# Performance work log

Hardware: AMD Instinct MI355X
Metric: run time of the kernel (lower is better)

The kernel has to match this reference:

```python
import jax, jax.numpy as jnp
import numpy as np
from jax import lax

T, B, I, H = 512, 128, 512, 1024  # seq_len, batch, n_input, n_hidden


def setup_inputs() -> dict:
    key = jax.random.key(0)
    ks = jax.random.split(key, 7)
    si, sh = I ** -0.5, H ** -0.5  # scaled init so tanh does not saturate
    return {
        "x":   jax.random.normal(ks[0], (T, B, I), jnp.float32),
        "Wi0": jax.random.normal(ks[1], (I, H), jnp.float32) * si,
        "Wh0": jax.random.normal(ks[2], (H, H), jnp.float32) * sh,
        "Ws0": jax.random.normal(ks[3], (I, H), jnp.float32) * si,
        "Wi1": jax.random.normal(ks[4], (H, H), jnp.float32) * sh,
        "Wh1": jax.random.normal(ks[5], (H, H), jnp.float32) * sh,
        "Ws1": jax.random.normal(ks[6], (I, H), jnp.float32) * si,
    }


def _wrnn_layer(pre, Wh):
    # pre: [L, B, H] precomputed non-recurrent projections (input-proj + scaled-input-proj)
    # h_t = tanh(pre[t] + h_{t-1} @ Wh)   -- true sequential recurrence
    def step(h, p):
        h = jnp.tanh(p + h @ Wh)
        return h, h
    h0 = jnp.zeros(pre.shape[1:], pre.dtype)
    _, out = lax.scan(step, h0, pre)
    return out  # [L, B, H]


def reference(x, Wi0, Wh0, Ws0, Wi1, Wh1, Ws1):
    # Layer 0: scale = 1, so scaled_x == x and input == x; index offset 0.
    # Hoist both non-recurrent matmuls into one big GEMM over all timesteps.
    pre0 = jnp.einsum('tbi,ih->tbh', x, Wi0 + Ws0)  # same as x@Wi0 + x@Ws0
    out0 = _wrnn_layer(pre0, Wh0)                   # [T, B, H]

    # Layer 1: scale = 2 moving average of x (length T-1); input = out0 at index i+1.
    sx1 = (x[:-1] + x[1:]) * 0.5                    # [T-1, B, I]
    pre1 = (jnp.einsum('tbh,hk->tbk', out0[1:], Wi1)
            + jnp.einsum('tbi,ih->tbh', sx1, Ws1))  # [T-1, B, H]
    out1 = _wrnn_layer(pre1, Wh1)                   # [T-1, B, H]

    return (out0, out1)
```

## Files before the change

### kernel.cpp

```cpp
#include <hip/hip_runtime.h>
#include <hip/hip_bf16.h>
#include <math.h>

#define T_ 512
#define B_ 128
#define I_ 512
#define H_ 1024

typedef __attribute__((ext_vector_type(8))) short short8;
typedef __attribute__((ext_vector_type(4))) float floatx4;

__device__ inline unsigned int f32_to_bf16_rne(float v) {
    unsigned int b = __builtin_bit_cast(unsigned int, v);
    b += 0x7FFFu + ((b >> 16) & 1u);
    return b >> 16;
}
__device__ inline float bf16_to_f32(unsigned int s) {
    unsigned int b = s << 16;
    return __builtin_bit_cast(float, b);
}
__device__ inline void split1(float v, short& hi, short& lo) {
    unsigned int h = f32_to_bf16_rne(v);
    float r = v - bf16_to_f32(h);
    unsigned int l = f32_to_bf16_rne(r);
    hi = (short)h;
    lo = (short)l;
}

__global__ void transpose_split_kernel(const float* __restrict__ in, const float* __restrict__ in2,
                                       short* __restrict__ outT_hi, short* __restrict__ outT_lo,
                                       int K, int N) {
    int total = K * N;
    int idx = blockIdx.x * blockDim.x + threadIdx.x;
    int stride = gridDim.x * blockDim.x;
    for (int i = idx; i < total; i += stride) {
        int n = i / K;
        int k = i - n * K;
        float v = in[(size_t)k * N + n];
        if (in2) v += in2[(size_t)k * N + n];
        short h, l;
        split1(v, h, l);
        outT_hi[i] = h;
        outT_lo[i] = l;
    }
}

__global__ __launch_bounds__(256) void gemm_split_kernel(const float* __restrict__ A,
                                                         const short* __restrict__ BT_hi,
                                                         const short* __restrict__ BT_lo,
                                                         float* __restrict__ C,
                                                         int K, int avg_off, int accumulate) {
    int tid = threadIdx.x;
    int wave = tid >> 6;
    int lane = tid & 63;
    int mbase = blockIdx.x * 64 + wave * 16;
    int nbase = blockIdx.y * 16;

    int arow = mbase + (lane & 15);
    int brow = nbase + (lane & 15);
    int koff = (lane >> 4) * 8;

    const float* ap = A + (size_t)arow * K + koff;
    const short* bph = BT_hi + (size_t)brow * K + koff;
    const short* bpl = BT_lo + (size_t)brow * K + koff;

    floatx4 acc = {0.f, 0.f, 0.f, 0.f};
    for (int k = 0; k < K; k += 32) {
        short8 ah, al, bh, bl;
        bh = *(const short8*)(bph + k);
        bl = *(const short8*)(bpl + k);
        #pragma unroll
        for (int j = 0; j < 8; ++j) {
            float v = ap[k + j];
            if (avg_off) v = 0.5f * (v + ap[k + j + avg_off]);
            short h, l;
            split1(v, h, l);
            ah[j] = h;
            al[j] = l;
        }
        acc = __builtin_amdgcn_mfma_f32_16x16x32_bf16(ah, bh, acc, 0, 0, 0);
        acc = __builtin_amdgcn_mfma_f32_16x16x32_bf16(al, bh, acc, 0, 0, 0);
        acc = __builtin_amdgcn_mfma_f32_16x16x32_bf16(ah, bl, acc, 0, 0, 0);
    }

    int rbase = mbase + ((lane >> 4) << 2);
    int c = nbase + (lane & 15);
    #pragma unroll
    for (int r = 0; r < 4; ++r) {
        size_t idx = (size_t)(rbase + r) * H_ + c;
        if (accumulate) C[idx] += acc[r];
        else            C[idx] = acc[r];
    }
}

__global__ __launch_bounds__(256) void step_kernel(const float* __restrict__ hprev,
                                                   const short* __restrict__ WhT_hi,
                                                   const short* __restrict__ WhT_lo,
                                                   const float* __restrict__ pre,
                                                   float* __restrict__ outf) {
    __shared__ float red[4][256];
    int tid = threadIdx.x;
    int wave = tid >> 6;
    int lane = tid & 63;
    int mbase = blockIdx.x * 16;
    int nbase = blockIdx.y * 16;

    floatx4 acc = {0.f, 0.f, 0.f, 0.f};
    if (hprev) {
        int arow = mbase + (lane & 15);
        int brow = nbase + (lane & 15);
        int koff = wave * 256 + (lane >> 4) * 8;
        const float* ap = hprev + (size_t)arow * H_ + koff;
        const short* bph = WhT_hi + (size_t)brow * H_ + koff;
        const short* bpl = WhT_lo + (size_t)brow * H_ + koff;
        #pragma unroll
        for (int k = 0; k < 256; k += 32) {
            short8 ah, al, bh, bl;
            bh = *(const short8*)(bph + k);
            bl = *(const short8*)(bpl + k);
            #pragma unroll
            for (int j = 0; j < 8; ++j) {
                short h, l;
                split1(ap[k + j], h, l);
                ah[j] = h;
                al[j] = l;
            }
            acc = __builtin_amdgcn_mfma_f32_16x16x32_bf16(ah, bh, acc, 0, 0, 0);
            acc = __builtin_amdgcn_mfma_f32_16x16x32_bf16(al, bh, acc, 0, 0, 0);
            acc = __builtin_amdgcn_mfma_f32_16x16x32_bf16(ah, bl, acc, 0, 0, 0);
        }
    }

    #pragma unroll
    for (int r = 0; r < 4; ++r)
        red[wave][r * 64 + lane] = acc[r];
    __syncthreads();

    if (tid < 64) {
        int rbase = mbase + ((lane >> 4) << 2);
        int c = nbase + (lane & 15);
        #pragma unroll
        for (int r = 0; r < 4; ++r) {
            float s = red[0][r * 64 + lane] + red[1][r * 64 + lane]
                    + red[2][r * 64 + lane] + red[3][r * 64 + lane];
            size_t idx = (size_t)(rbase + r) * H_ + c;
            outf[idx] = tanhf(pre[idx] + s);
        }
    }
}


extern "C" void kernel_launch(void* const* d_in, const int* in_sizes, int n_in,
                              void* d_out, int out_size, void* d_ws, size_t ws_size,
                              hipStream_t stream) {
    const float* x   = (const float*)d_in[0];
    const float* Wi0 = (const float*)d_in[1];
    const float* Wh0 = (const float*)d_in[2];
    const float* Ws0 = (const float*)d_in[3];
    const float* Wi1 = (const float*)d_in[4];
    const float* Wh1 = (const float*)d_in[5];
    const float* Ws1 = (const float*)d_in[6];
    float* out = (float*)d_out;
    char* ws = (char*)d_ws;

    const size_t BH = (size_t)B_ * H_;
    const size_t OUT1_OFF = (size_t)T_ * BH;

    const size_t MB = 1048576ull;
    float* pre      = (float*)(ws + 0);
    short* W0sumT_h = (short*)(ws + 256 * MB);
    short* W0sumT_l = (short*)(ws + 257 * MB);
    short* Wh0T_h   = (short*)(ws + 258 * MB);
    short* Wh0T_l   = (short*)(ws + 260 * MB);
    short* Wi1T_h   = (short*)(ws + 262 * MB);
    short* Wi1T_l   = (short*)(ws + 264 * MB);
    short* Wh1T_h   = (short*)(ws + 266 * MB);
    short* Wh1T_l   = (short*)(ws + 268 * MB);
    short* Ws1T_h   = (short*)(ws + 270 * MB);
    short* Ws1T_l   = (short*)(ws + 271 * MB);

    transpose_split_kernel<<<dim3((I_ * H_ + 255) / 256), 256, 0, stream>>>(Wi0, Ws0, W0sumT_h, W0sumT_l, I_, H_);
    transpose_split_kernel<<<dim3((H_ * H_ + 255) / 256), 256, 0, stream>>>(Wh0, nullptr, Wh0T_h, Wh0T_l, H_, H_);
    transpose_split_kernel<<<dim3((H_ * H_ + 255) / 256), 256, 0, stream>>>(Wi1, nullptr, Wi1T_h, Wi1T_l, H_, H_);
    transpose_split_kernel<<<dim3((H_ * H_ + 255) / 256), 256, 0, stream>>>(Wh1, nullptr, Wh1T_h, Wh1T_l, H_, H_);
    transpose_split_kernel<<<dim3((I_ * H_ + 255) / 256), 256, 0, stream>>>(Ws1, nullptr, Ws1T_h, Ws1T_l, I_, H_);

    gemm_split_kernel<<<dim3(65536 / 64, H_ / 16), 256, 0, stream>>>(
        x, W0sumT_h, W0sumT_l, pre, I_, 0, 0);

    for (int t = 0; t < T_; ++t) {
        const float* hp = (t == 0) ? nullptr : (out + (size_t)(t - 1) * BH);
        step_kernel<<<dim3(8, H_ / 16), 256, 0, stream>>>(
            hp, Wh0T_h, Wh0T_l, pre + (size_t)t * BH, out + (size_t)t * BH);
    }

    gemm_split_kernel<<<dim3(65408 / 64, H_ / 16), 256, 0, stream>>>(
        out + BH, Wi1T_h, Wi1T_l, pre, H_, 0, 0);
    gemm_split_kernel<<<dim3(65408 / 64, H_ / 16), 256, 0, stream>>>(
        x, Ws1T_h, Ws1T_l, pre, I_, B_ * I_, 1);

    for (int t = 0; t < T_ - 1; ++t) {
        const float* hp = (t == 0) ? nullptr : (out + OUT1_OFF + (size_t)(t - 1) * BH);
        step_kernel<<<dim3(8, H_ / 16), 256, 0, stream>>>(
            hp, Wh1T_h, Wh1T_l, pre + (size_t)t * BH, out + OUT1_OFF + (size_t)t * BH);
    }
}
```

Baseline: 33.27 ms.

## Replace per-timestep launches with persistent recurrence kernel using atomic group barriers

Replaces the 1023 per-timestep step_kernel launches with one persistent kernel per layer. Each of 512 blocks keeps its 16-column slice of the recurrent weight in LDS and waits on per-batch-row-group atomic counters before consuming the previous step's hidden state. The hidden state is stored pre-split into bf16 hi/lo double buffers, so the split work is not redone for every tile. This removes launch overhead and repeated weight reloads, but relies on all 512 blocks being co-resident, since a block that is not resident would deadlock the spin-waits.

```diff
diff --git a/kernel.cpp b/kernel.cpp
--- a/kernel.cpp
+++ b/kernel.cpp
@@ -1,5 +1,4 @@
 #include <hip/hip_runtime.h>
-#include <hip/hip_bf16.h>
 #include <math.h>
 
 #define T_ 512
@@ -93,59 +92,102 @@
     }
 }
 
-__global__ __launch_bounds__(256) void step_kernel(const float* __restrict__ hprev,
-                                                   const short* __restrict__ WhT_hi,
-                                                   const short* __restrict__ WhT_lo,
-                                                   const float* __restrict__ pre,
-                                                   float* __restrict__ outf) {
+#define GRP_NB 64
+
+__global__ __launch_bounds__(256) void recur_kernel(const short* __restrict__ WhT_hi,
+                                                    const short* __restrict__ WhT_lo,
+                                                    const float* __restrict__ pre,
+                                                    float* __restrict__ outf,
+                                                    short* __restrict__ h_hi,
+                                                    short* __restrict__ h_lo,
+                                                    unsigned int* __restrict__ cnt,
+                                                    int nsteps) {
+    __shared__ short bh_lds[16][1032];
+    __shared__ short bl_lds[16][1032];
     __shared__ float red[4][256];
-    int tid = threadIdx.x;
-    int wave = tid >> 6;
-    int lane = tid & 63;
-    int mbase = blockIdx.x * 16;
-    int nbase = blockIdx.y * 16;
-
-    floatx4 acc = {0.f, 0.f, 0.f, 0.f};
-    if (hprev) {
-        int arow = mbase + (lane & 15);
-        int brow = nbase + (lane & 15);
-        int koff = wave * 256 + (lane >> 4) * 8;
-        const float* ap = hprev + (size_t)arow * H_ + koff;
-        const short* bph = WhT_hi + (size_t)brow * H_ + koff;
-        const short* bpl = WhT_lo + (size_t)brow * H_ + koff;
+
+    const int tid = threadIdx.x;
+    const int wave = tid >> 6;
+    const int lane = tid & 63;
+    const int mb = blockIdx.x & 7;
+    const int nb = blockIdx.x >> 3;
+    const int mbase = mb * 16;
+    const int nbase = nb * 16;
+    const size_t BH = (size_t)B_ * H_;
+
+    for (int i = tid; i < 2048; i += 256) {
+        int n = i >> 7;
+        int k8 = (i & 127) << 3;
+        *(short8*)&bh_lds[n][k8] = *(const short8*)(WhT_hi + (size_t)(nbase + n) * H_ + k8);
+        *(short8*)&bl_lds[n][k8] = *(const short8*)(WhT_lo + (size_t)(nbase + n) * H_ + k8);
+    }
+    __syncthreads();
+
+    const int arow = mbase + (lane & 15);
+    const int brow = lane & 15;
+    const int koff = wave * 256 + ((lane >> 4) << 3);
+
+    const int erow = mbase + ((lane >> 4) << 2);
+    const int ecol = nbase + (lane & 15);
+
+    unsigned int* cg = cnt + mb * T_;
+
+    for (int t = 0; t < nsteps; ++t) {
+        float pv[4];
+        if (tid < 64) {
+            #pragma unroll
+            for (int r = 0; r < 4; ++r)
+                pv[r] = pre[(size_t)t * BH + (size_t)(erow + r) * H_ + ecol];
+        }
+
+        floatx4 acc = {0.f, 0.f, 0.f, 0.f};
+        if (t > 0) {
+            if (tid == 0) {
+                while (__hip_atomic_load(&cg[t - 1], __ATOMIC_ACQUIRE,
+                                         __HIP_MEMORY_SCOPE_AGENT) < GRP_NB)
+                    __builtin_amdgcn_s_sleep(1);
+            }
+            __syncthreads();
+
+            const size_t hoff = ((t - 1) & 1) ? BH : 0;
+            const short* aph = h_hi + hoff + (size_t)arow * H_ + koff;
+            const short* apl = h_lo + hoff + (size_t)arow * H_ + koff;
+            #pragma unroll
+            for (int k = 0; k < 256; k += 32) {
+                short8 ah = *(const short8*)(aph + k);
+                short8 al = *(const short8*)(apl + k);
+                short8 bh = *(const short8*)&bh_lds[brow][koff + k];
+                short8 bl = *(const short8*)&bl_lds[brow][koff + k];
+                acc = __builtin_amdgcn_mfma_f32_16x16x32_bf16(ah, bh, acc, 0, 0, 0);
+                acc = __builtin_amdgcn_mfma_f32_16x16x32_bf16(al, bh, acc, 0, 0, 0);
+                acc = __builtin_amdgcn_mfma_f32_16x16x32_bf16(ah, bl, acc, 0, 0, 0);
+            }
+        }
+
         #pragma unroll
-        for (int k = 0; k < 256; k += 32) {
-            short8 ah, al, bh, bl;
-            bh = *(const short8*)(bph + k);
-            bl = *(const short8*)(bpl + k);
+        for (int r = 0; r < 4; ++r)
+            red[wave][r * 64 + lane] = acc[r];
+        __syncthreads();
+
+        if (tid < 64) {
+            const size_t hoff = (t & 1) ? BH : 0;
             #pragma unroll
-            for (int j = 0; j < 8; ++j) {
-                short h, l;
-                split1(ap[k + j], h, l);
-                ah[j] = h;
-                al[j] = l;
+            for (int r = 0; r < 4; ++r) {
+                float s = red[0][r * 64 + lane] + red[1][r * 64 + lane]
+                        + red[2][r * 64 + lane] + red[3][r * 64 + lane];
+                float v = tanhf(pv[r] + s);
+                size_t idx = (size_t)(erow + r) * H_ + ecol;
+                outf[(size_t)t * BH + idx] = v;
+                short hh, ll;
+                split1(v, hh, ll);
+                h_hi[hoff + idx] = hh;
+                h_lo[hoff + idx] = ll;
             }
-            acc = __builtin_amdgcn_mfma_f32_16x16x32_bf16(ah, bh, acc, 0, 0, 0);
-            acc = __builtin_amdgcn_mfma_f32_16x16x32_bf16(al, bh, acc, 0, 0, 0);
-            acc = __builtin_amdgcn_mfma_f32_16x16x32_bf16(ah, bl, acc, 0, 0, 0);
-        }
-    }
-
-    #pragma unroll
-    for (int r = 0; r < 4; ++r)
-        red[wave][r * 64 + lane] = acc[r];
-    __syncthreads();
-
-    if (tid < 64) {
-        int rbase = mbase + ((lane >> 4) << 2);
-        int c = nbase + (lane & 15);
-        #pragma unroll
-        for (int r = 0; r < 4; ++r) {
-            float s = red[0][r * 64 + lane] + red[1][r * 64 + lane]
-                    + red[2][r * 64 + lane] + red[3][r * 64 + lane];
-            size_t idx = (size_t)(rbase + r) * H_ + c;
-            outf[idx] = tanhf(pre[idx] + s);
-        }
+            __threadfence();
+        }
+        __syncthreads();
+        if (tid == 0)
+            __hip_atomic_fetch_add(&cg[t], 1u, __ATOMIC_RELEASE, __HIP_MEMORY_SCOPE_AGENT);
     }
 }
 
@@ -178,6 +220,9 @@
     short* Wh1T_l   = (short*)(ws + 268 * MB);
     short* Ws1T_h   = (short*)(ws + 270 * MB);
     short* Ws1T_l   = (short*)(ws + 271 * MB);
+    short* h_hi     = (short*)(ws + 272 * MB);
+    short* h_lo     = (short*)(ws + 272 * MB + 524288);
+    unsigned int* cnt = (unsigned int*)(ws + 273 * MB);
 
     transpose_split_kernel<<<dim3((I_ * H_ + 255) / 256), 256, 0, stream>>>(Wi0, Ws0, W0sumT_h, W0sumT_l, I_, H_);
     transpose_split_kernel<<<dim3((H_ * H_ + 255) / 256), 256, 0, stream>>>(Wh0, nullptr, Wh0T_h, Wh0T_l, H_, H_);
@@ -188,20 +233,16 @@
     gemm_split_kernel<<<dim3(65536 / 64, H_ / 16), 256, 0, stream>>>(
         x, W0sumT_h, W0sumT_l, pre, I_, 0, 0);
 
-    for (int t = 0; t < T_; ++t) {
-        const float* hp = (t == 0) ? nullptr : (out + (size_t)(t - 1) * BH);
-        step_kernel<<<dim3(8, H_ / 16), 256, 0, stream>>>(
-            hp, Wh0T_h, Wh0T_l, pre + (size_t)t * BH, out + (size_t)t * BH);
-    }
+    hipMemsetAsync(cnt, 0, 8 * T_ * sizeof(unsigned int), stream);
+    recur_kernel<<<dim3(512), 256, 0, stream>>>(
+        Wh0T_h, Wh0T_l, pre, out, h_hi, h_lo, cnt, T_);
 
     gemm_split_kernel<<<dim3(65408 / 64, H_ / 16), 256, 0, stream>>>(
         out + BH, Wi1T_h, Wi1T_l, pre, H_, 0, 0);
     gemm_split_kernel<<<dim3(65408 / 64, H_ / 16), 256, 0, stream>>>(
         x, Ws1T_h, Ws1T_l, pre, I_, B_ * I_, 1);
 
-    for (int t = 0; t < T_ - 1; ++t) {
-        const float* hp = (t == 0) ? nullptr : (out + OUT1_OFF + (size_t)(t - 1) * BH);
-        step_kernel<<<dim3(8, H_ / 16), 256, 0, stream>>>(
-            hp, Wh1T_h, Wh1T_l, pre + (size_t)t * BH, out + OUT1_OFF + (size_t)t * BH);
-    }
-}
+    hipMemsetAsync(cnt, 0, 8 * T_ * sizeof(unsigned int), stream);
+    recur_kernel<<<dim3(512), 256, 0, stream>>>(
+        Wh1T_h, Wh1T_l, pre, out + OUT1_OFF, h_hi, h_lo, cnt, T_ - 1);
+}
```

Result: slower. 59.02 ms (+77.4%).
